# Optimization experiments

Hardware: AMD Instinct MI355X
Metric: run time of the kernel (lower is better)

The kernel has to match this reference:

```python
import jax, jax.numpy as jnp
import numpy as np

N = 50000
E = 640000
DIM_NODE = 128
DIM_HIDDEN = 128
DIM_FFN = 512
NUM_CLASSES = 10
NUM_GRAPHS = 128
NEG_SLOPE = 0.2


def setup_inputs() -> dict:
    key = jax.random.key(0)
    ks = jax.random.split(key, 24)
    g = lambda k, shape: jax.random.normal(k, shape, dtype=jnp.float32) * 0.05
    inp = {
        "x": jax.random.normal(ks[0], (N, DIM_NODE), dtype=jnp.float32),
        "edge_index": jax.random.randint(ks[1], (2, E), 0, N, dtype=jnp.int64),
        "batch": jnp.sort(jax.random.randint(ks[2], (N,), 0, NUM_GRAPHS, dtype=jnp.int64)),
        # GATConv 1: dim_node -> dim_hidden (heads=1)
        "W1": g(ks[3], (DIM_NODE, DIM_HIDDEN)),
        "as1": g(ks[4], (DIM_HIDDEN,)), "ad1": g(ks[5], (DIM_HIDDEN,)),
        "b1": g(ks[6], (DIM_HIDDEN,)),
        # GATConv 2
        "W2": g(ks[7], (DIM_HIDDEN, DIM_HIDDEN)),
        "as2": g(ks[8], (DIM_HIDDEN,)), "ad2": g(ks[9], (DIM_HIDDEN,)),
        "b2": g(ks[10], (DIM_HIDDEN,)),
        # GATConv 3
        "W3": g(ks[11], (DIM_HIDDEN, DIM_HIDDEN)),
        "as3": g(ks[12], (DIM_HIDDEN,)), "ad3": g(ks[13], (DIM_HIDDEN,)),
        "b3": g(ks[14], (DIM_HIDDEN,)),
        # FFN head
        "Wf1": g(ks[15], (DIM_HIDDEN, DIM_FFN)), "bf1": g(ks[16], (DIM_FFN,)),
        "Wf2": g(ks[17], (DIM_FFN, DIM_FFN)), "bf2": g(ks[18], (DIM_FFN,)),
        "Wf3": g(ks[19], (DIM_FFN, NUM_CLASSES)), "bf3": g(ks[20], (NUM_CLASSES,)),
    }
    return inp


def _gat_conv(x, src, dst, W, a_src, a_dst, bias):
    # x: [N, Fin]; src/dst: [E'] (self-loops included)
    h = x @ W                                  # [N, H]
    alpha_src = h @ a_src                      # [N]
    alpha_dst = h @ a_dst                      # [N]
    logits = jax.nn.leaky_relu(alpha_src[src] + alpha_dst[dst], NEG_SLOPE)  # [E']
    # segment softmax over incoming edges of each dst node
    m = jax.ops.segment_max(logits, dst, num_segments=N)
    ex = jnp.exp(logits - m[dst])
    denom = jax.ops.segment_sum(ex, dst, num_segments=N)
    alpha = ex / (denom[dst] + 1e-16)          # [E']
    out = jax.ops.segment_sum(alpha[:, None] * h[src], dst, num_segments=N)
    return out + bias


def reference(x, edge_index, batch, W1, as1, ad1, b1, W2, as2, ad2, b2,
              W3, as3, ad3, b3, Wf1, bf1, Wf2, bf2, Wf3, bf3):
    # PyG GATConv adds self-loops by default
    loops = jnp.arange(N, dtype=edge_index.dtype)
    src = jnp.concatenate([edge_index[0], loops])
    dst = jnp.concatenate([edge_index[1], loops])

    h = jax.nn.relu(_gat_conv(x, src, dst, W1, as1, ad1, b1))
    h = jax.nn.relu(_gat_conv(h, src, dst, W2, as2, ad2, b2))
    h = jax.nn.relu(_gat_conv(h, src, dst, W3, as3, ad3, b3))

    # global mean pool per graph
    sums = jax.ops.segment_sum(h, batch, num_segments=NUM_GRAPHS)
    cnts = jax.ops.segment_sum(jnp.ones((N,), h.dtype), batch, num_segments=NUM_GRAPHS)
    pooled = sums / jnp.maximum(cnts, 1.0)[:, None]   # [G, H]

    # FFN head (dropout is identity in eval)
    z = jax.nn.relu(pooled @ Wf1 + bf1)
    z = jax.nn.relu(z @ Wf2 + bf2)
    return z @ Wf3 + bf3                               # [G, num_classes]
```

## Files before the change

### kernel.cpp

```cpp
#include <hip/hip_runtime.h>

#define N_NODES 50000
#define N_EDGES 640000
#define TOT_E (N_EDGES + N_NODES)
#define NB 196
#define BCAP 4608
#define EPW 4096
#define NG 128
#define NCLS 10
#define NEG 0.2f
#define PCHUNK 50

typedef unsigned int u32;
typedef unsigned short u16;
typedef __attribute__((ext_vector_type(8))) short s16x8;
typedef __attribute__((ext_vector_type(4))) float f32x4;

__device__ inline u32 bf16rne(float f) {
  u32 u = __float_as_uint(f);
  return (u + 0x7FFFu + ((u >> 16) & 1u)) >> 16;
}
__device__ inline float bf2f(u16 v) { return __uint_as_float((u32)v << 16); }

__global__ __launch_bounds__(256) void prep_kernel(int* __restrict__ bcur,
                                                   float* __restrict__ psum,
                                                   const float* __restrict__ W0,
                                                   const float* __restrict__ W1,
                                                   const float* __restrict__ W2,
                                                   u16* __restrict__ Wt) {
  int i = blockIdx.x * 256 + threadIdx.x;
  if (i < NB) bcur[i] = 0;
  if (i < NG * 128) psum[i] = 0.f;
  if (i < 3 * 128 * 128) {
    int l = i >> 14, c = (i >> 7) & 127, k = i & 127;
    const float* W = (l == 0) ? W0 : ((l == 1) ? W1 : W2);
    Wt[i] = (u16)bf16rne(W[k * 128 + c]);
  }
}

__global__ __launch_bounds__(256) void scatter_kernel(const int* __restrict__ ei,
                                                      int* __restrict__ bcur,
                                                      u32* __restrict__ ebuf) {
  __shared__ int hist[NB], basee[NB], lcur[NB];
  int t = threadIdx.x;
  for (int b = t; b < NB; b += 256) hist[b] = 0;
  __syncthreads();
  int e0 = blockIdx.x * EPW;
  int e1 = min(TOT_E, e0 + EPW);
  for (int e = e0 + t; e < e1; e += 256) {
    int d = (e < N_EDGES) ? ei[N_EDGES + e] : (e - N_EDGES);
    atomicAdd(&hist[d >> 8], 1);
  }
  __syncthreads();
  for (int b = t; b < NB; b += 256) {
    int c = hist[b];
    basee[b] = (c > 0) ? atomicAdd(&bcur[b], c) : 0;
    lcur[b] = 0;
  }
  __syncthreads();
  for (int e = e0 + t; e < e1; e += 256) {
    int d, s;
    if (e < N_EDGES) { d = ei[N_EDGES + e]; s = ei[e]; }
    else { d = e - N_EDGES; s = d; }
    int b = d >> 8;
    int r = basee[b] + atomicAdd(&lcur[b], 1);
    if (r < BCAP) ebuf[(size_t)b * BCAP + r] = ((u32)d << 16) | (u32)s;
  }
}

__global__ __launch_bounds__(256) void degscan_kernel(const int* __restrict__ bcur,
                                                      const u32* __restrict__ ebuf,
                                                      int* __restrict__ rowptr,
                                                      int* __restrict__ bsum) {
  __shared__ int cnt[256], s[256];
  int b = blockIdx.x, t = threadIdx.x;
  cnt[t] = 0; __syncthreads();
  int n = min(bcur[b], BCAP);
  const u32* eb = ebuf + (size_t)b * BCAP;
  for (int i = t; i < n; i += 256) atomicAdd(&cnt[(eb[i] >> 16) & 255], 1);
  __syncthreads();
  int v = cnt[t];
  s[t] = v; __syncthreads();
  for (int off = 1; off < 256; off <<= 1) {
    int tmp = (t >= off) ? s[t - off] : 0;
    __syncthreads();
    s[t] += tmp;
    __syncthreads();
  }
  int node = (b << 8) + t;
  if (node < N_NODES) rowptr[node] = s[t] - v;
  if (t == 255) bsum[b] = s[255];
}

__global__ void scanB(const int* __restrict__ bsum, int* __restrict__ bofs) {
  __shared__ int s[256];
  int t = threadIdx.x;
  int v = (t < NB) ? bsum[t] : 0;
  s[t] = v; __syncthreads();
  for (int off = 1; off < 256; off <<= 1) {
    int tmp = (t >= off) ? s[t - off] : 0;
    __syncthreads();
    s[t] += tmp;
    __syncthreads();
  }
  if (t < NB) bofs[t] = s[t] - v;
}

__global__ void scanC(int* __restrict__ rowptr, const int* __restrict__ bofs) {
  int i = blockIdx.x * 256 + threadIdx.x;
  if (i < N_NODES) rowptr[i] += bofs[i >> 8];
  if (i == 0) rowptr[N_NODES] = TOT_E;
}

__global__ __launch_bounds__(256) void fill2_kernel(const int* __restrict__ bcur,
                                                    const u32* __restrict__ ebuf,
                                                    const int* __restrict__ rowptr,
                                                    u16* __restrict__ col) {
  __shared__ int cur[256];
  int b = blockIdx.x, t = threadIdx.x;
  int node = (b << 8) + t;
  cur[t] = (node < N_NODES) ? rowptr[node] : 0;
  __syncthreads();
  int n = min(bcur[b], BCAP);
  const u32* eb = ebuf + (size_t)b * BCAP;
  for (int i = t; i < n; i += 256) {
    u32 p = eb[i];
    int pos = atomicAdd(&cur[(p >> 16) & 255], 1);
    col[pos] = (u16)(p & 0xFFFFu);
  }
}

template <bool CVT>
__global__ __launch_bounds__(64) void gemm_mfma(const void* __restrict__ Xin,
                                                const u16* __restrict__ Wt,
                                                const float* __restrict__ avs,
                                                const float* __restrict__ avd,
                                                u16* __restrict__ Hb,
                                                float* __restrict__ as_out,
                                                float* __restrict__ ad_out) {
  __shared__ u16 st[16 * 128];
  int lane = threadIdx.x;
  int m0 = blockIdx.x * 16;
  int ar = lane & 15, kg = lane >> 4;
  f32x4 acc[8];
#pragma unroll
  for (int n = 0; n < 8; n++) acc[n] = (f32x4){0.f, 0.f, 0.f, 0.f};
#pragma unroll
  for (int ks = 0; ks < 4; ks++) {
    s16x8 a;
    if (CVT) {
      const float* xr = (const float*)Xin + (size_t)(m0 + ar) * 128 + ks * 32 + kg * 8;
      float4 f0 = *(const float4*)xr;
      float4 f1 = *(const float4*)(xr + 4);
      a[0] = (short)bf16rne(f0.x); a[1] = (short)bf16rne(f0.y);
      a[2] = (short)bf16rne(f0.z); a[3] = (short)bf16rne(f0.w);
      a[4] = (short)bf16rne(f1.x); a[5] = (short)bf16rne(f1.y);
      a[6] = (short)bf16rne(f1.z); a[7] = (short)bf16rne(f1.w);
    } else {
      a = *(const s16x8*)((const u16*)Xin + (size_t)(m0 + ar) * 128 + ks * 32 + kg * 8);
    }
#pragma unroll
    for (int n = 0; n < 8; n++) {
      s16x8 b = *(const s16x8*)(Wt + (size_t)(n * 16 + ar) * 128 + ks * 32 + kg * 8);
      acc[n] = __builtin_amdgcn_mfma_f32_16x16x32_bf16(a, b, acc[n], 0, 0, 0);
    }
  }
  float avsv[8], advv[8];
#pragma unroll
  for (int n = 0; n < 8; n++) { avsv[n] = avs[n * 16 + ar]; advv[n] = avd[n * 16 + ar]; }
#pragma unroll
  for (int reg = 0; reg < 4; reg++) {
    float ps = 0.f, pd = 0.f;
#pragma unroll
    for (int n = 0; n < 8; n++) {
      ps = fmaf(acc[n][reg], avsv[n], ps);
      pd = fmaf(acc[n][reg], advv[n], pd);
    }
#pragma unroll
    for (int off = 1; off < 16; off <<= 1) {
      ps += __shfl_xor(ps, off, 64);
      pd += __shfl_xor(pd, off, 64);
    }
    if (ar == 0) {
      int row = m0 + kg * 4 + reg;
      as_out[row] = ps; ad_out[row] = pd;
    }
  }
#pragma unroll
  for (int n = 0; n < 8; n++)
#pragma unroll
    for (int reg = 0; reg < 4; reg++)
      st[(kg * 4 + reg) * 128 + n * 16 + ar] = (u16)bf16rne(acc[n][reg]);
  __syncthreads();
#pragma unroll
  for (int i = 0; i < 4; i++) {
    int u4 = i * 64 + lane;
    int r = u4 >> 4;
    int c8 = (u4 & 15) * 8;
    *(uint4*)(Hb + (size_t)(m0 + r) * 128 + c8) = *(const uint4*)&st[r * 128 + c8];
  }
}

__global__ __launch_bounds__(256) void agg_kernel(
    const u16* __restrict__ Hb, const float* __restrict__ asv,
    const float* __restrict__ adv, const int* __restrict__ rowptr,
    const u16* __restrict__ col, const float* __restrict__ bias,
    u16* __restrict__ Ob) {
  int gid = blockIdx.x * blockDim.x + threadIdx.x;
  int node = gid >> 6;
  if (node >= N_NODES) return;
  int lane = threadIdx.x & 63;
  int q = lane >> 4;
  int li = lane & 15;
  int r0 = rowptr[node], r1 = rowptr[node + 1];
  float ad = adv[node];
  float acc[8];
#pragma unroll
  for (int k = 0; k < 8; k++) acc[k] = 0.f;
  float den = 0.f;

  for (int base = r0; base < r1; base += 64) {
    int cnt = min(64, r1 - base);
    int s_l = 0; float ex_l = 0.f;
    if (lane < cnt) {
      s_l = (int)col[base + lane];
      float tt = asv[s_l] + ad;
      tt = (tt > 0.f) ? tt : NEG * tt;
      ex_l = __expf(tt);
    }
    float d = ex_l;
#pragma unroll
    for (int off = 32; off; off >>= 1) d += __shfl_xor(d, off, 64);
    den += d;

    int j = 0;
    for (; j + 8 <= cnt; j += 8) {
      int i0 = j + q, i1 = j + 4 + q;
      int s0 = __shfl(s_l, i0, 64); float e0 = __shfl(ex_l, i0, 64);
      int s1 = __shfl(s_l, i1, 64); float e1 = __shfl(ex_l, i1, 64);
      uint4 h0 = *(const uint4*)(Hb + (size_t)s0 * 128 + li * 8);
      uint4 h1 = *(const uint4*)(Hb + (size_t)s1 * 128 + li * 8);
      u32 w0[4] = {h0.x, h0.y, h0.z, h0.w};
      u32 w1[4] = {h1.x, h1.y, h1.z, h1.w};
#pragma unroll
      for (int k = 0; k < 4; k++) {
        acc[2 * k]     = fmaf(e0, __uint_as_float(w0[k] << 16), acc[2 * k]);
        acc[2 * k + 1] = fmaf(e0, __uint_as_float(w0[k] & 0xFFFF0000u), acc[2 * k + 1]);
      }
#pragma unroll
      for (int k = 0; k < 4; k++) {
        acc[2 * k]     = fmaf(e1, __uint_as_float(w1[k] << 16), acc[2 * k]);
        acc[2 * k + 1] = fmaf(e1, __uint_as_float(w1[k] & 0xFFFF0000u), acc[2 * k + 1]);
      }
    }
    for (; j < cnt; j += 4) {
      int i0 = j + q;
      int s0 = __shfl(s_l, i0, 64); float e0 = __shfl(ex_l, i0, 64);
      if (i0 < cnt) {
        uint4 h0 = *(const uint4*)(Hb + (size_t)s0 * 128 + li * 8);
        u32 w0[4] = {h0.x, h0.y, h0.z, h0.w};
#pragma unroll
        for (int k = 0; k < 4; k++) {
          acc[2 * k]     = fmaf(e0, __uint_as_float(w0[k] << 16), acc[2 * k]);
          acc[2 * k + 1] = fmaf(e0, __uint_as_float(w0[k] & 0xFFFF0000u), acc[2 * k + 1]);
        }
      }
    }
  }
#pragma unroll
  for (int k = 0; k < 8; k++) {
    acc[k] += __shfl_xor(acc[k], 16, 64);
    acc[k] += __shfl_xor(acc[k], 32, 64);
  }

  if (q == 0) {
    float inv = 1.f / (den + 1e-16f);
    float4 b0 = *(const float4*)(bias + li * 8);
    float4 b1 = *(const float4*)(bias + li * 8 + 4);
    float o[8];
    o[0] = fmaxf(fmaf(acc[0], inv, b0.x), 0.f);
    o[1] = fmaxf(fmaf(acc[1], inv, b0.y), 0.f);
    o[2] = fmaxf(fmaf(acc[2], inv, b0.z), 0.f);
    o[3] = fmaxf(fmaf(acc[3], inv, b0.w), 0.f);
    o[4] = fmaxf(fmaf(acc[4], inv, b1.x), 0.f);
    o[5] = fmaxf(fmaf(acc[5], inv, b1.y), 0.f);
    o[6] = fmaxf(fmaf(acc[6], inv, b1.z), 0.f);
    o[7] = fmaxf(fmaf(acc[7], inv, b1.w), 0.f);
    uint4 pb;
    pb.x = bf16rne(o[0]) | (bf16rne(o[1]) << 16);
    pb.y = bf16rne(o[2]) | (bf16rne(o[3]) << 16);
    pb.z = bf16rne(o[4]) | (bf16rne(o[5]) << 16);
    pb.w = bf16rne(o[6]) | (bf16rne(o[7]) << 16);
    *(uint4*)(Ob + (size_t)node * 128 + li * 8) = pb;
  }
}

__global__ void pool_kernel(const u16* __restrict__ Hb, const int* __restrict__ batch,
                            float* __restrict__ psum) {
  int t = threadIdx.x;
  int start = blockIdx.x * PCHUNK;
  int end = min(N_NODES, start + PCHUNK);
  if (start >= end) return;
  int cur = batch[start];
  float acc = 0.f;
  for (int i = start; i < end; ++i) {
    int g = batch[i];
    if (g != cur) {
      atomicAdd(&psum[cur * 128 + t], acc);
      acc = 0.f; cur = g;
    }
    acc += bf2f(Hb[(size_t)i * 128 + t]);
  }
  atomicAdd(&psum[cur * 128 + t], acc);
}

__device__ inline int lbound(const int* b, int n, int v) {
  int lo = 0, hi = n;
  while (lo < hi) { int m = (lo + hi) >> 1; if (b[m] < v) lo = m + 1; else hi = m; }
  return lo;
}

__global__ __launch_bounds__(512) void ffn_fused(const float* __restrict__ psum,
                                                 const int* __restrict__ batch,
                                                 const float* __restrict__ Wf1,
                                                 const float* __restrict__ bf1,
                                                 const float* __restrict__ Wf2,
                                                 const float* __restrict__ bf2,
                                                 const float* __restrict__ Wf3,
                                                 const float* __restrict__ bf3,
                                                 float* __restrict__ out) {
  __shared__ float prow[128], z1s[512], z2s[512];
  __shared__ float cnt_s;
  int g = blockIdx.x, t = threadIdx.x;
  if (t == 0) {
    int lo = lbound(batch, N_NODES, g), hi = lbound(batch, N_NODES, g + 1);
    cnt_s = fmaxf((float)(hi - lo), 1.f);
  }
  __syncthreads();
  if (t < 128) prow[t] = psum[g * 128 + t] / cnt_s;
  __syncthreads();
  float a1 = bf1[t];
  for (int k = 0; k < 128; ++k) a1 = fmaf(prow[k], Wf1[k * 512 + t], a1);
  z1s[t] = fmaxf(a1, 0.f);
  __syncthreads();
  float a2 = bf2[t];
  for (int k = 0; k < 512; ++k) a2 = fmaf(z1s[k], Wf2[k * 512 + t], a2);
  z2s[t] = fmaxf(a2, 0.f);
  __syncthreads();
  if (t < 160) {
    int c = t >> 4, l16 = t & 15;
    float p = 0.f;
#pragma unroll
    for (int j = 0; j < 32; ++j) {
      int k = l16 + 16 * j;
      p = fmaf(z2s[k], Wf3[k * NCLS + c], p);
    }
    p += __shfl_xor(p, 8, 16);
    p += __shfl_xor(p, 4, 16);
    p += __shfl_xor(p, 2, 16);
    p += __shfl_xor(p, 1, 16);
    if (l16 == 0) out[g * NCLS + c] = p + bf3[c];
  }
}

extern "C" void kernel_launch(void* const* d_in, const int* in_sizes, int n_in,
                              void* d_out, int out_size, void* d_ws, size_t ws_size,
                              hipStream_t stream) {
  const float* x   = (const float*)d_in[0];
  const int*   ei  = (const int*)d_in[1];
  const int*   bat = (const int*)d_in[2];
  const float* W[3]  = {(const float*)d_in[3], (const float*)d_in[7],  (const float*)d_in[11]};
  const float* As[3] = {(const float*)d_in[4], (const float*)d_in[8],  (const float*)d_in[12]};
  const float* Ad[3] = {(const float*)d_in[5], (const float*)d_in[9],  (const float*)d_in[13]};
  const float* B[3]  = {(const float*)d_in[6], (const float*)d_in[10], (const float*)d_in[14]};
  const float* Wf1 = (const float*)d_in[15]; const float* bf1 = (const float*)d_in[16];
  const float* Wf2 = (const float*)d_in[17]; const float* bf2 = (const float*)d_in[18];
  const float* Wf3 = (const float*)d_in[19]; const float* bf3 = (const float*)d_in[20];
  float* out = (float*)d_out;

  size_t off = 0;
  auto carve = [&](size_t bytes) {
    void* p = (char*)d_ws + off;
    off += (bytes + 255) & ~(size_t)255;
    return p;
  };
  u16*   Ab0    = (u16*)carve((size_t)N_NODES * 128 * 2);
  u16*   Ab1    = (u16*)carve((size_t)N_NODES * 128 * 2);
  u16*   Hb     = (u16*)carve((size_t)N_NODES * 128 * 2);
  u16*   Wt     = (u16*)carve((size_t)3 * 128 * 128 * 2);
  float* as_    = (float*)carve((size_t)N_NODES * 4);
  float* ad_    = (float*)carve((size_t)N_NODES * 4);
  int*   rowptr = (int*)carve((size_t)(N_NODES + 1) * 4);
  u16*   col    = (u16*)carve((size_t)TOT_E * 2);
  u32*   ebuf   = (u32*)carve((size_t)NB * BCAP * 4);
  int*   bcur   = (int*)carve(NB * 4);
  int*   bsum   = (int*)carve(256 * 4);
  int*   bofs   = (int*)carve(256 * 4);
  float* psum   = (float*)carve(NG * 128 * 4);

  prep_kernel<<<256, 256, 0, stream>>>(bcur, psum, W[0], W[1], W[2], Wt);

  int sgrid = (TOT_E + EPW - 1) / EPW;
  scatter_kernel<<<sgrid, 256, 0, stream>>>(ei, bcur, ebuf);
  degscan_kernel<<<NB, 256, 0, stream>>>(bcur, ebuf, rowptr, bsum);
  scanB<<<1, 256, 0, stream>>>(bsum, bofs);
  scanC<<<NB, 256, 0, stream>>>(rowptr, bofs);
  fill2_kernel<<<NB, 256, 0, stream>>>(bcur, ebuf, rowptr, col);

  int node_waves_grid = (N_NODES * 64 + 255) / 256;
  gemm_mfma<true><<<3125, 64, 0, stream>>>(x, Wt, As[0], Ad[0], Hb, as_, ad_);
  agg_kernel<<<node_waves_grid, 256, 0, stream>>>(Hb, as_, ad_, rowptr, col, B[0], Ab0);
  gemm_mfma<false><<<3125, 64, 0, stream>>>(Ab0, Wt + 16384, As[1], Ad[1], Hb, as_, ad_);
  agg_kernel<<<node_waves_grid, 256, 0, stream>>>(Hb, as_, ad_, rowptr, col, B[1], Ab1);
  gemm_mfma<false><<<3125, 64, 0, stream>>>(Ab1, Wt + 32768, As[2], Ad[2], Hb, as_, ad_);
  agg_kernel<<<node_waves_grid, 256, 0, stream>>>(Hb, as_, ad_, rowptr, col, B[2], Ab0);

  pool_kernel<<<(N_NODES + PCHUNK - 1) / PCHUNK, 128, 0, stream>>>(Ab0, bat, psum);
  ffn_fused<<<NG, 512, 0, stream>>>(psum, bat, Wf1, bf1, Wf2, bf2, Wf3, bf3, out);
}
```

Baseline: 241.1 us.

## Replace global CSR scan with per-bucket offsets and fuse mean pooling into FFN

```diff
diff --git a/kernel.cpp b/kernel.cpp
--- a/kernel.cpp
+++ b/kernel.cpp
@@ -9,7 +9,6 @@
 #define NG 128
 #define NCLS 10
 #define NEG 0.2f
-#define PCHUNK 50
 
 typedef unsigned int u32;
 typedef unsigned short u16;
@@ -23,14 +22,12 @@
 __device__ inline float bf2f(u16 v) { return __uint_as_float((u32)v << 16); }
 
 __global__ __launch_bounds__(256) void prep_kernel(int* __restrict__ bcur,
-                                                   float* __restrict__ psum,
                                                    const float* __restrict__ W0,
                                                    const float* __restrict__ W1,
                                                    const float* __restrict__ W2,
                                                    u16* __restrict__ Wt) {
   int i = blockIdx.x * 256 + threadIdx.x;
   if (i < NB) bcur[i] = 0;
-  if (i < NG * 128) psum[i] = 0.f;
   if (i < 3 * 128 * 128) {
     int l = i >> 14, c = (i >> 7) & 127, k = i & 127;
     const float* W = (l == 0) ? W0 : ((l == 1) ? W1 : W2);
@@ -68,11 +65,11 @@
   }
 }
 
-__global__ __launch_bounds__(256) void degscan_kernel(const int* __restrict__ bcur,
+__global__ __launch_bounds__(256) void degfill_kernel(const int* __restrict__ bcur,
                                                       const u32* __restrict__ ebuf,
-                                                      int* __restrict__ rowptr,
-                                                      int* __restrict__ bsum) {
-  __shared__ int cnt[256], s[256];
+                                                      u32* __restrict__ rldeg,
+                                                      u16* __restrict__ col) {
+  __shared__ int cnt[256], s[256], cur[256];
   int b = blockIdx.x, t = threadIdx.x;
   cnt[t] = 0; __syncthreads();
   int n = min(bcur[b], BCAP);
@@ -87,46 +84,16 @@
     s[t] += tmp;
     __syncthreads();
   }
+  int rl = s[t] - v;
   int node = (b << 8) + t;
-  if (node < N_NODES) rowptr[node] = s[t] - v;
-  if (t == 255) bsum[b] = s[255];
-}
-
-__global__ void scanB(const int* __restrict__ bsum, int* __restrict__ bofs) {
-  __shared__ int s[256];
-  int t = threadIdx.x;
-  int v = (t < NB) ? bsum[t] : 0;
-  s[t] = v; __syncthreads();
-  for (int off = 1; off < 256; off <<= 1) {
-    int tmp = (t >= off) ? s[t - off] : 0;
-    __syncthreads();
-    s[t] += tmp;
-    __syncthreads();
-  }
-  if (t < NB) bofs[t] = s[t] - v;
-}
-
-__global__ void scanC(int* __restrict__ rowptr, const int* __restrict__ bofs) {
-  int i = blockIdx.x * 256 + threadIdx.x;
-  if (i < N_NODES) rowptr[i] += bofs[i >> 8];
-  if (i == 0) rowptr[N_NODES] = TOT_E;
-}
-
-__global__ __launch_bounds__(256) void fill2_kernel(const int* __restrict__ bcur,
-                                                    const u32* __restrict__ ebuf,
-                                                    const int* __restrict__ rowptr,
-                                                    u16* __restrict__ col) {
-  __shared__ int cur[256];
-  int b = blockIdx.x, t = threadIdx.x;
-  int node = (b << 8) + t;
-  cur[t] = (node < N_NODES) ? rowptr[node] : 0;
-  __syncthreads();
-  int n = min(bcur[b], BCAP);
-  const u32* eb = ebuf + (size_t)b * BCAP;
+  if (node < N_NODES) rldeg[node] = ((u32)rl << 16) | (u32)v;
+  cur[t] = rl;
+  __syncthreads();
+  u16* cb = col + (size_t)b * BCAP;
   for (int i = t; i < n; i += 256) {
     u32 p = eb[i];
     int pos = atomicAdd(&cur[(p >> 16) & 255], 1);
-    col[pos] = (u16)(p & 0xFFFFu);
+    cb[pos] = (u16)(p & 0xFFFFu);
   }
 }
 
@@ -203,7 +170,7 @@
 
 __global__ __launch_bounds__(256) void agg_kernel(
     const u16* __restrict__ Hb, const float* __restrict__ asv,
-    const float* __restrict__ adv, const int* __restrict__ rowptr,
+    const float* __restrict__ adv, const u32* __restrict__ rldeg,
     const u16* __restrict__ col, const float* __restrict__ bias,
     u16* __restrict__ Ob) {
   int gid = blockIdx.x * blockDim.x + threadIdx.x;
@@ -212,7 +179,9 @@
   int lane = threadIdx.x & 63;
   int q = lane >> 4;
   int li = lane & 15;
-  int r0 = rowptr[node], r1 = rowptr[node + 1];
+  u32 rd = rldeg[node];
+  int r0 = (node >> 8) * BCAP + (int)(rd >> 16);
+  int r1 = r0 + (int)(rd & 0xFFFFu);
   float ad = adv[node];
   float acc[8];
 #pragma unroll
@@ -295,32 +264,13 @@
   }
 }
 
-__global__ void pool_kernel(const u16* __restrict__ Hb, const int* __restrict__ batch,
-                            float* __restrict__ psum) {
-  int t = threadIdx.x;
-  int start = blockIdx.x * PCHUNK;
-  int end = min(N_NODES, start + PCHUNK);
-  if (start >= end) return;
-  int cur = batch[start];
-  float acc = 0.f;
-  for (int i = start; i < end; ++i) {
-    int g = batch[i];
-    if (g != cur) {
-      atomicAdd(&psum[cur * 128 + t], acc);
-      acc = 0.f; cur = g;
-    }
-    acc += bf2f(Hb[(size_t)i * 128 + t]);
-  }
-  atomicAdd(&psum[cur * 128 + t], acc);
-}
-
 __device__ inline int lbound(const int* b, int n, int v) {
   int lo = 0, hi = n;
   while (lo < hi) { int m = (lo + hi) >> 1; if (b[m] < v) lo = m + 1; else hi = m; }
   return lo;
 }
 
-__global__ __launch_bounds__(512) void ffn_fused(const float* __restrict__ psum,
+__global__ __launch_bounds__(512) void ffn_fused(const u16* __restrict__ Ab,
                                                  const int* __restrict__ batch,
                                                  const float* __restrict__ Wf1,
                                                  const float* __restrict__ bf1,
@@ -329,15 +279,18 @@
                                                  const float* __restrict__ Wf3,
                                                  const float* __restrict__ bf3,
                                                  float* __restrict__ out) {
+  __shared__ float part[512];
   __shared__ float prow[128], z1s[512], z2s[512];
-  __shared__ float cnt_s;
   int g = blockIdx.x, t = threadIdx.x;
-  if (t == 0) {
-    int lo = lbound(batch, N_NODES, g), hi = lbound(batch, N_NODES, g + 1);
-    cnt_s = fmaxf((float)(hi - lo), 1.f);
-  }
-  __syncthreads();
-  if (t < 128) prow[t] = psum[g * 128 + t] / cnt_s;
+  int lo = lbound(batch, N_NODES, g), hi = lbound(batch, N_NODES, g + 1);
+  float cnt = fmaxf((float)(hi - lo), 1.f);
+  int dim = t & 127, rg = t >> 7;
+  float a = 0.f;
+  for (int row = lo + rg; row < hi; row += 4)
+    a += bf2f(Ab[(size_t)row * 128 + dim]);
+  part[t] = a;
+  __syncthreads();
+  if (t < 128) prow[t] = (part[t] + part[t + 128] + part[t + 256] + part[t + 384]) / cnt;
   __syncthreads();
   float a1 = bf1[t];
   for (int k = 0; k < 128; ++k) a1 = fmaf(prow[k], Wf1[k * 512 + t], a1);
@@ -390,31 +343,24 @@
   u16*   Wt     = (u16*)carve((size_t)3 * 128 * 128 * 2);
   float* as_    = (float*)carve((size_t)N_NODES * 4);
   float* ad_    = (float*)carve((size_t)N_NODES * 4);
-  int*   rowptr = (int*)carve((size_t)(N_NODES + 1) * 4);
-  u16*   col    = (u16*)carve((size_t)TOT_E * 2);
+  u32*   rldeg  = (u32*)carve((size_t)N_NODES * 4);
+  u16*   col    = (u16*)carve((size_t)NB * BCAP * 2);
   u32*   ebuf   = (u32*)carve((size_t)NB * BCAP * 4);
   int*   bcur   = (int*)carve(NB * 4);
-  int*   bsum   = (int*)carve(256 * 4);
-  int*   bofs   = (int*)carve(256 * 4);
-  float* psum   = (float*)carve(NG * 128 * 4);
-
-  prep_kernel<<<256, 256, 0, stream>>>(bcur, psum, W[0], W[1], W[2], Wt);
+
+  prep_kernel<<<192, 256, 0, stream>>>(bcur, W[0], W[1], W[2], Wt);
 
   int sgrid = (TOT_E + EPW - 1) / EPW;
   scatter_kernel<<<sgrid, 256, 0, stream>>>(ei, bcur, ebuf);
-  degscan_kernel<<<NB, 256, 0, stream>>>(bcur, ebuf, rowptr, bsum);
-  scanB<<<1, 256, 0, stream>>>(bsum, bofs);
-  scanC<<<NB, 256, 0, stream>>>(rowptr, bofs);
-  fill2_kernel<<<NB, 256, 0, stream>>>(bcur, ebuf, rowptr, col);
+  degfill_kernel<<<NB, 256, 0, stream>>>(bcur, ebuf, rldeg, col);
 
   int node_waves_grid = (N_NODES * 64 + 255) / 256;
   gemm_mfma<true><<<3125, 64, 0, stream>>>(x, Wt, As[0], Ad[0], Hb, as_, ad_);
-  agg_kernel<<<node_waves_grid, 256, 0, stream>>>(Hb, as_, ad_, rowptr, col, B[0], Ab0);
+  agg_kernel<<<node_waves_grid, 256, 0, stream>>>(Hb, as_, ad_, rldeg, col, B[0], Ab0);
   gemm_mfma<false><<<3125, 64, 0, stream>>>(Ab0, Wt + 16384, As[1], Ad[1], Hb, as_, ad_);
-  agg_kernel<<<node_waves_grid, 256, 0, stream>>>(Hb, as_, ad_, rowptr, col, B[1], Ab1);
+  agg_kernel<<<node_waves_grid, 256, 0, stream>>>(Hb, as_, ad_, rldeg, col, B[1], Ab1);
   gemm_mfma<false><<<3125, 64, 0, stream>>>(Ab1, Wt + 32768, As[2], Ad[2], Hb, as_, ad_);
-  agg_kernel<<<node_waves_grid, 256, 0, stream>>>(Hb, as_, ad_, rowptr, col, B[2], Ab0);
-
-  pool_kernel<<<(N_NODES + PCHUNK - 1) / PCHUNK, 128, 0, stream>>>(Ab0, bat, psum);
-  ffn_fused<<<NG, 512, 0, stream>>>(psum, bat, Wf1, bf1, Wf2, bf2, Wf3, bf3, out);
-}
+  agg_kernel<<<node_waves_grid, 256, 0, stream>>>(Hb, as_, ad_, rldeg, col, B[2], Ab0);
+
+  ffn_fused<<<NG, 512, 0, stream>>>(Ab0, bat, Wf1, bf1, Wf2, bf2, Wf3, bf3, out);
+}
```

After: 238.7 us. No clear change (-1.0%).
